# Performance work log

Measured on AMD Instinct MI355X. Metric: run time of the kernel, lower is better.

## Reference

```python
import jax, jax.numpy as jnp
import numpy as np

N = 4096
C = 8192
D = 64
MARGIN = 0.1
ALPHA = 32.0


def setup_inputs() -> dict:
    key = jax.random.key(0)
    k1, k2, k3, k4 = jax.random.split(key, 4)
    embeddings = jax.random.normal(k1, (N, D), dtype=jnp.float32)
    labels = jax.random.randint(k2, (N,), 0, C)
    # kaiming_normal_(mode='fan_out') on a (C, D) tensor -> std = sqrt(2/C)
    mean_proxies = jax.random.normal(k3, (C, D), dtype=jnp.float32) * np.sqrt(2.0 / C)
    log_variance_proxies = jax.random.normal(k4, (C, D), dtype=jnp.float32) * np.sqrt(2.0 / C)
    return {
        "embeddings": embeddings,
        "labels": labels,
        "mean_proxies": mean_proxies,
        "log_variance_proxies": log_variance_proxies,
    }


def _mls_scores(e, mu, logvar):
    """score[i,j] = -0.5 * sum_d[(e_id - mu_jd)^2 * exp(-logvar_jd) + logvar_jd].
    Expanded into GEMMs to avoid materializing the (N, C, D) broadcast tensor."""
    inv_var = jnp.exp(-logvar)                                  # (C, D)
    e2_term = (e * e) @ inv_var.T                               # (N, C)
    cross = e @ (mu * inv_var).T                                # (N, C)
    const = jnp.sum(mu * mu * inv_var + logvar, axis=1)         # (C,)
    return -0.5 * (e2_term - 2.0 * cross + const[None, :])      # (N, C)


def reference(embeddings, labels, mean_proxies, log_variance_proxies):
    score_mat = _mls_scores(embeddings, mean_proxies, log_variance_proxies)  # (N, C)
    pos_mask = jax.nn.one_hot(labels, C, dtype=score_mat.dtype)              # (N, C)

    pos_e = -ALPHA * (score_mat - MARGIN)
    neg_e = ALPHA * (score_mat + MARGIN)
    m = jnp.max(pos_e)  # NOTE: original code uses max(pos_exp) for BOTH terms
    pos_exp = jnp.exp(pos_e - m)
    neg_exp = jnp.exp(neg_e - m)

    counts = jnp.sum(pos_mask, axis=0)                   # (C,)
    num_valid = jnp.sum(counts != 0).astype(score_mat.dtype)

    pos_sim_sum = jnp.sum(jnp.where(pos_mask == 1, pos_exp, 0.0), axis=0)  # (C,)
    neg_sim_sum = jnp.sum(jnp.where(pos_mask == 0, neg_exp, 0.0), axis=0)  # (C,)

    pos_term = jnp.sum(jnp.log1p(pos_sim_sum) + m) / num_valid
    neg_term = jnp.sum(jnp.log1p(neg_sim_sum) + m) / C
    return pos_term + neg_term
```

## Files before the change

### kernel.cpp

```cpp
#include <hip/hip_runtime.h>
#include <hip/hip_bf16.h>
#include <math.h>


#define N_EMB 4096
#define C_CLS 8192
#define D_DIM 64
#define K_DIM 128

#define S2_F    23.083120654223414f
#define B2_F     4.616624130844683f
#define NEGC2_F  9.233248261689366f
#define LN2_F    0.6931471805599453f

typedef __attribute__((ext_vector_type(8))) __bf16 bf16x8;
typedef __attribute__((ext_vector_type(4))) __bf16 bf16x4;
typedef __attribute__((ext_vector_type(16))) float f32x16;
typedef __attribute__((ext_vector_type(4))) int i32x4;

__device__ __forceinline__ void async_ld16(void* lds, const void* g) {
  __builtin_amdgcn_global_load_lds(
      (__attribute__((address_space(1))) void*)g,
      (__attribute__((address_space(3))) void*)lds, 16, 0, 0);
}

__global__ void k_prep(const float* __restrict__ emb,
                       const float* __restrict__ mp,
                       const float* __restrict__ lvp,
                       __bf16* __restrict__ wsA,
                       __bf16* __restrict__ wsB,
                       float* __restrict__ constv) {
  const int wave = (int)((blockIdx.x * blockDim.x + threadIdx.x) >> 6);
  const int lane = threadIdx.x & 63;
  const int sub = lane >> 4, q = lane & 15;
  const int row = wave * 4 + sub;
  if (row < N_EMB) {
    float4 e4 = *(const float4*)&emb[row * D_DIM + q * 4];
    bf16x4 sq = {(__bf16)(e4.x * e4.x), (__bf16)(e4.y * e4.y),
                 (__bf16)(e4.z * e4.z), (__bf16)(e4.w * e4.w)};
    bf16x4 ev = {(__bf16)e4.x, (__bf16)e4.y, (__bf16)e4.z, (__bf16)e4.w};
    *(bf16x4*)&wsA[row * K_DIM + q * 4] = sq;
    *(bf16x4*)&wsA[row * K_DIM + D_DIM + q * 4] = ev;
  } else {
    const int j = row - N_EMB;
    float4 mu4 = *(const float4*)&mp[j * D_DIM + q * 4];
    float4 lv4 = *(const float4*)&lvp[j * D_DIM + q * 4];
    float iv0 = __expf(-lv4.x), iv1 = __expf(-lv4.y);
    float iv2 = __expf(-lv4.z), iv3 = __expf(-lv4.w);
    bf16x4 ivv = {(__bf16)iv0, (__bf16)iv1, (__bf16)iv2, (__bf16)iv3};
    bf16x4 mv = {(__bf16)(-2.0f * mu4.x * iv0), (__bf16)(-2.0f * mu4.y * iv1),
                 (__bf16)(-2.0f * mu4.z * iv2), (__bf16)(-2.0f * mu4.w * iv3)};
    *(bf16x4*)&wsB[j * K_DIM + q * 4] = ivv;
    *(bf16x4*)&wsB[j * K_DIM + D_DIM + q * 4] = mv;
    float t = fmaf(mu4.x * mu4.x, iv0, lv4.x)
            + fmaf(mu4.y * mu4.y, iv1, lv4.y)
            + fmaf(mu4.z * mu4.z, iv2, lv4.z)
            + fmaf(mu4.w * mu4.w, iv3, lv4.w);
    #pragma unroll
    for (int s = 8; s >= 1; s >>= 1) t += __shfl_xor(t, s);
    if (q == 0) constv[j] = t;
  }
}

__global__ __launch_bounds__(256, 2) void k_main(
    const __bf16* __restrict__ wsA, const __bf16* __restrict__ wsB,
    const float* __restrict__ constv, const int* __restrict__ labels,
    float* __restrict__ wsM, float* __restrict__ wsP, float* __restrict__ wsN) {
  __shared__ __align__(16) char As[32768];
  __shared__ __align__(16) char Bs[32768];

  const int tid = threadIdx.x;
  const int rb = blockIdx.x & 31;
  const int cb = blockIdx.x >> 5;

  const char* Ag = (const char*)(wsA + (size_t)rb * 128 * K_DIM);
  const char* Bg = (const char*)(wsB + (size_t)cb * 128 * K_DIM);
  #pragma unroll
  for (int it = 0; it < 8; ++it) {
    int L = it * 256 + tid;
    int r = L >> 4, cs = L & 15;
    int goff = r * 256 + ((cs ^ (r & 15)) << 4);
    async_ld16(As + L * 16, Ag + goff);
  }
  #pragma unroll
  for (int it = 0; it < 8; ++it) {
    int L = it * 256 + tid;
    int r = L >> 4, cs = L & 15;
    int goff = r * 256 + ((cs ^ (r & 15)) << 4);
    async_ld16(Bs + L * 16, Bg + goff);
  }
  int lab_r = 0; float cv_r = 0.f;
  if (tid < 128) {
    lab_r = labels[rb * 128 + tid];
    cv_r  = constv[cb * 128 + tid];
  }
  __syncthreads();

  const int wv = tid >> 6, lane = tid & 63;
  const int wr = wv >> 1, wc = wv & 1;
  const int l31 = lane & 31, kg = lane >> 5;
  const int l15 = lane & 15;

  f32x16 acc[2][2];
  #pragma unroll
  for (int mi = 0; mi < 2; ++mi)
    #pragma unroll
    for (int ni = 0; ni < 2; ++ni)
      #pragma unroll
      for (int r = 0; r < 16; ++r) acc[mi][ni][r] = 0.f;

  #pragma unroll
  for (int kk = 0; kk < 8; ++kk) {
    const int c = kk * 2 + kg;
    const int cofs = (c ^ l15) << 4;
    bf16x8 af[2], bfr[2];
    #pragma unroll
    for (int mi = 0; mi < 2; ++mi)
      af[mi] = *(const bf16x8*)(As + (wr * 64 + mi * 32 + l31) * 256 + cofs);
    #pragma unroll
    for (int ni = 0; ni < 2; ++ni)
      bfr[ni] = *(const bf16x8*)(Bs + (wc * 64 + ni * 32 + l31) * 256 + cofs);
    #pragma unroll
    for (int mi = 0; mi < 2; ++mi)
      #pragma unroll
      for (int ni = 0; ni < 2; ++ni)
        acc[mi][ni] = __builtin_amdgcn_mfma_f32_32x32x16_bf16(
            af[mi], bfr[ni], acc[mi][ni], 0, 0, 0);
  }

  __syncthreads();
  float* colred = (float*)As;
  int* labels_s = (int*)(As + 3072);
  float* pc_s   = (float*)(As + 3584);
  if (tid < 128) {
    labels_s[tid] = lab_r;
    pc_s[tid] = fmaf(S2_F, cv_r, B2_F);
  }
  __syncthreads();

  i32x4 labv[2][4];
  #pragma unroll
  for (int mi = 0; mi < 2; ++mi)
    #pragma unroll
    for (int g = 0; g < 4; ++g)
      labv[mi][g] = *(const i32x4*)&labels_s[wr * 64 + mi * 32 + 4 * kg + 8 * g];

  #pragma unroll
  for (int ni = 0; ni < 2; ++ni) {
    const int col_local = wc * 64 + ni * 32 + l31;
    const int gcol = cb * 128 + col_local;
    const float pcv = pc_s[col_local];
    float lmax = -1e30f;
    #pragma unroll
    for (int mi = 0; mi < 2; ++mi)
      #pragma unroll
      for (int r = 0; r < 16; ++r) {
        float pe = fmaf(S2_F, acc[mi][ni][r], pcv);
        acc[mi][ni][r] = pe;
        lmax = fmaxf(lmax, pe);
      }
    lmax = fmaxf(lmax, __shfl_xor(lmax, 32));
    const float negb = NEGC2_F - lmax;
    float ps = 0.f, ns = 0.f;
    #pragma unroll
    for (int mi = 0; mi < 2; ++mi)
      #pragma unroll
      for (int r = 0; r < 16; ++r) {
        float pe = acc[mi][ni][r];
        bool match = (labv[mi][r >> 2][r & 3] == gcol);
        float a = match ? (pe - lmax) : (negb - pe);
        float ex = exp2f(a);
        ps += match ? ex : 0.f;
        ns += match ? 0.f : ex;
      }
    ps += __shfl_xor(ps, 32);
    ns += __shfl_xor(ns, 32);
    if (kg == 0) {
      float* cr = &colred[(wr * 128 + col_local) * 3];
      cr[0] = lmax; cr[1] = ps; cr[2] = ns;
    }
  }
  __syncthreads();
  if (tid < 128) {
    const float* c0 = &colred[(0 * 128 + tid) * 3];
    const float* c1 = &colred[(1 * 128 + tid) * 3];
    float M = fmaxf(c0[0], c1[0]);
    float s0 = exp2f(c0[0] - M), s1 = exp2f(c1[0] - M);
    int gcol = cb * 128 + tid;
    wsM[rb * C_CLS + gcol] = M;
    wsP[rb * C_CLS + gcol] = fmaf(c0[1], s0, c1[1] * s1);
    wsN[rb * C_CLS + gcol] = fmaf(c0[2], s0, c1[2] * s1);
  }
}

__global__ __launch_bounds__(256) void k_red1(
    const float* __restrict__ wsM, const float* __restrict__ wsP,
    const float* __restrict__ wsN, const int* __restrict__ labels,
    float* __restrict__ Mcol, float* __restrict__ Pcol,
    float* __restrict__ Ncol, int* __restrict__ nvp) {
  __shared__ float red[8][32][3];
  __shared__ int fl[32];
  const int tid = threadIdx.x;
  const int col = tid & 31, part = tid >> 5;
  const int bx = blockIdx.x;
  const int j = bx * 32 + col;

  if (tid < 32) fl[tid] = 0;

  float m4[4];
  float M = -1e30f;
  #pragma unroll
  for (int r = 0; r < 4; ++r) {
    m4[r] = wsM[(part * 4 + r) * C_CLS + j];
    M = fmaxf(M, m4[r]);
  }
  float ps = 0.f, ns = 0.f;
  #pragma unroll
  for (int r = 0; r < 4; ++r) {
    float s = exp2f(m4[r] - M);
    ps = fmaf(wsP[(part * 4 + r) * C_CLS + j], s, ps);
    ns = fmaf(wsN[(part * 4 + r) * C_CLS + j], s, ns);
  }
  red[part][col][0] = M; red[part][col][1] = ps; red[part][col][2] = ns;
  __syncthreads();

  #pragma unroll
  for (int it = 0; it < 4; ++it) {
    int4 lb = ((const int4*)labels)[it * 256 + tid];
    if ((lb.x >> 5) == bx) fl[lb.x & 31] = 1;
    if ((lb.y >> 5) == bx) fl[lb.y & 31] = 1;
    if ((lb.z >> 5) == bx) fl[lb.z & 31] = 1;
    if ((lb.w >> 5) == bx) fl[lb.w & 31] = 1;
  }

  if (part == 0) {
    float Mx = -1e30f;
    #pragma unroll
    for (int p = 0; p < 8; ++p) Mx = fmaxf(Mx, red[p][col][0]);
    float P = 0.f, Nn = 0.f;
    #pragma unroll
    for (int p = 0; p < 8; ++p) {
      float s = exp2f(red[p][col][0] - Mx);
      P = fmaf(red[p][col][1], s, P);
      Nn = fmaf(red[p][col][2], s, Nn);
    }
    Mcol[j] = Mx; Pcol[j] = P; Ncol[j] = Nn;
  }
  __syncthreads();
  if (tid < 64) {
    int f = (tid < 32) ? fl[tid] : 0;
    #pragma unroll
    for (int s = 32; s >= 1; s >>= 1) f += __shfl_xor(f, s);
    if (tid == 0) nvp[bx] = f;
  }
}

__global__ __launch_bounds__(1024) void k_fin(
    const float* __restrict__ Mcol, const float* __restrict__ Pcol,
    const float* __restrict__ Ncol, const int* __restrict__ nvp,
    float* __restrict__ out) {
  __shared__ float sA[16], sB[16];
  __shared__ int sI[16];
  const int tid = threadIdx.x;
  const int wv = tid >> 6, lane = tid & 63;

  float colMv[8], colPv[8], colNv[8];
  #pragma unroll
  for (int k = 0; k < 8; ++k) {
    int i = k * 1024 + tid;
    colMv[k] = Mcol[i]; colPv[k] = Pcol[i]; colNv[k] = Ncol[i];
  }
  int nv = (tid < 256) ? nvp[tid] : 0;

  float gm = -1e30f;
  #pragma unroll
  for (int k = 0; k < 8; ++k) gm = fmaxf(gm, colMv[k]);
  #pragma unroll
  for (int s = 32; s >= 1; s >>= 1) {
    gm = fmaxf(gm, __shfl_xor(gm, s));
    nv += __shfl_xor(nv, s);
  }
  if (lane == 0) { sA[wv] = gm; sI[wv] = nv; }
  __syncthreads();
  if (tid == 0) {
    float mm = -1e30f; int n = 0;
    #pragma unroll
    for (int k = 0; k < 16; ++k) { mm = fmaxf(mm, sA[k]); n += sI[k]; }
    sA[0] = mm; sI[0] = n;
  }
  __syncthreads();
  const float m = sA[0];
  const int num_valid = sI[0];
  __syncthreads();
  float pt = 0.f, nt = 0.f;
  #pragma unroll
  for (int k = 0; k < 8; ++k) {
    float s = exp2f(colMv[k] - m);
    pt += log1pf(colPv[k] * s);
    nt += log1pf(colNv[k] * s);
  }
  #pragma unroll
  for (int s = 32; s >= 1; s >>= 1) {
    pt += __shfl_xor(pt, s);
    nt += __shfl_xor(nt, s);
  }
  if (lane == 0) { sA[wv] = pt; sB[wv] = nt; }
  __syncthreads();
  if (tid == 0) {
    float sp = 0.f, sn = 0.f;
    #pragma unroll
    for (int k = 0; k < 16; ++k) { sp += sA[k]; sn += sB[k]; }
    const float mn = m * LN2_F;
    out[0] = (sp + (float)C_CLS * mn) / (float)num_valid
           + (sn + (float)C_CLS * mn) / (float)C_CLS;
  }
}

extern "C" void kernel_launch(void* const* d_in, const int* in_sizes, int n_in,
                              void* d_out, int out_size, void* d_ws, size_t ws_size,
                              hipStream_t stream) {
  const float* emb    = (const float*)d_in[0];
  const int*   labels = (const int*)d_in[1];
  const float* mp     = (const float*)d_in[2];
  const float* lvp    = (const float*)d_in[3];
  float* out = (float*)d_out;

  char* ws = (char*)d_ws;
  __bf16* wsA   = (__bf16*)ws;
  __bf16* wsB   = (__bf16*)(ws + (1u << 20));
  float* constv = (float*)(ws + 3u * (1u << 20));
  float* wsM    = (float*)(ws + 3u * (1u << 20) + (1u << 15));
  float* wsP    = wsM + 32 * C_CLS;
  float* wsN    = wsP + 32 * C_CLS;
  float* Mcol   = wsN + 32 * C_CLS;
  float* Pcol   = Mcol + C_CLS;
  float* Ncol   = Pcol + C_CLS;
  int*   nvp    = (int*)(Ncol + C_CLS);

  hipLaunchKernelGGL(k_prep, dim3(768), dim3(256), 0, stream,
                     emb, mp, lvp, wsA, wsB, constv);
  hipLaunchKernelGGL(k_main, dim3((N_EMB / 128) * (C_CLS / 128)), dim3(256), 0, stream,
                     wsA, wsB, constv, labels, wsM, wsP, wsN);
  hipLaunchKernelGGL(k_red1, dim3(256), dim3(256), 0, stream,
                     wsM, wsP, wsN, labels, Mcol, Pcol, Ncol, nvp);
  hipLaunchKernelGGL(k_fin, dim3(1), dim3(1024), 0, stream,
                     Mcol, Pcol, Ncol, nvp, out);
}
```

Before: 104.5 us.

## Process four column blocks per workgroup reusing the A tile, use raw v_exp

Each k_main workgroup now loops over four consecutive 128-column class blocks while keeping its 128-row A tile resident in LDS, reloading only B per block. The next B tile is issued asynchronously after the MFMA loop, before the epilogue, so it can overlap with the exp/reduction work. Labels and per-column constants are loaded straight into registers instead of being staged through LDS. exp2f is replaced by raw v_exp_f32 inline asm, and the negative term is computed for every element with the matching element subtracted back out. The grid shrinks fourfold to 512 blocks, which lowers parallelism on a large GPU and increases register pressure. The inline v_exp_f32 also skips the denormal range handling that exp2f provides.

```diff
diff --git a/kernel.cpp b/kernel.cpp
--- a/kernel.cpp
+++ b/kernel.cpp
@@ -7,6 +7,7 @@
 #define C_CLS 8192
 #define D_DIM 64
 #define K_DIM 128
+#define NCB 4
 
 #define S2_F    23.083120654223414f
 #define B2_F     4.616624130844683f
@@ -22,6 +23,12 @@
   __builtin_amdgcn_global_load_lds(
       (__attribute__((address_space(1))) void*)g,
       (__attribute__((address_space(3))) void*)lds, 16, 0, 0);
+}
+
+__device__ __forceinline__ float fexp2(float x) {
+  float r;
+  asm("v_exp_f32 %0, %1" : "=v"(r) : "v"(x));
+  return r;
 }
 
 __global__ void k_prep(const float* __restrict__ emb,
@@ -68,13 +75,14 @@
     float* __restrict__ wsM, float* __restrict__ wsP, float* __restrict__ wsN) {
   __shared__ __align__(16) char As[32768];
   __shared__ __align__(16) char Bs[32768];
+  __shared__ float colred[2][128][3];
 
   const int tid = threadIdx.x;
-  const int rb = blockIdx.x & 31;
-  const int cb = blockIdx.x >> 5;
+  const int rb  = blockIdx.x & 31;
+  const int cbg = blockIdx.x >> 5;
 
   const char* Ag = (const char*)(wsA + (size_t)rb * 128 * K_DIM);
-  const char* Bg = (const char*)(wsB + (size_t)cb * 128 * K_DIM);
+  const char* Bgb = (const char*)(wsB + (size_t)(cbg * NCB) * 128 * K_DIM);
   #pragma unroll
   for (int it = 0; it < 8; ++it) {
     int L = it * 256 + tid;
@@ -87,109 +95,121 @@
     int L = it * 256 + tid;
     int r = L >> 4, cs = L & 15;
     int goff = r * 256 + ((cs ^ (r & 15)) << 4);
-    async_ld16(Bs + L * 16, Bg + goff);
-  }
-  int lab_r = 0; float cv_r = 0.f;
-  if (tid < 128) {
-    lab_r = labels[rb * 128 + tid];
-    cv_r  = constv[cb * 128 + tid];
-  }
-  __syncthreads();
+    async_ld16(Bs + L * 16, Bgb + goff);
+  }
 
   const int wv = tid >> 6, lane = tid & 63;
   const int wr = wv >> 1, wc = wv & 1;
   const int l31 = lane & 31, kg = lane >> 5;
   const int l15 = lane & 15;
 
-  f32x16 acc[2][2];
+  i32x4 labv[2][4];
   #pragma unroll
   for (int mi = 0; mi < 2; ++mi)
     #pragma unroll
+    for (int g = 0; g < 4; ++g)
+      labv[mi][g] = *(const i32x4*)&labels[rb * 128 + wr * 64 + mi * 32 +
+                                           4 * kg + 8 * g];
+  float cvv[NCB][2];
+  #pragma unroll
+  for (int cbi = 0; cbi < NCB; ++cbi)
+    #pragma unroll
     for (int ni = 0; ni < 2; ++ni)
-      #pragma unroll
-      for (int r = 0; r < 16; ++r) acc[mi][ni][r] = 0.f;
-
-  #pragma unroll
-  for (int kk = 0; kk < 8; ++kk) {
-    const int c = kk * 2 + kg;
-    const int cofs = (c ^ l15) << 4;
-    bf16x8 af[2], bfr[2];
+      cvv[cbi][ni] = constv[(cbg * NCB + cbi) * 128 + wc * 64 + ni * 32 + l31];
+
+  __syncthreads();
+
+  #pragma unroll
+  for (int cbi = 0; cbi < NCB; ++cbi) {
+    const int cb = cbg * NCB + cbi;
+
+    f32x16 acc[2][2];
     #pragma unroll
     for (int mi = 0; mi < 2; ++mi)
-      af[mi] = *(const bf16x8*)(As + (wr * 64 + mi * 32 + l31) * 256 + cofs);
-    #pragma unroll
-    for (int ni = 0; ni < 2; ++ni)
-      bfr[ni] = *(const bf16x8*)(Bs + (wc * 64 + ni * 32 + l31) * 256 + cofs);
-    #pragma unroll
-    for (int mi = 0; mi < 2; ++mi)
       #pragma unroll
       for (int ni = 0; ni < 2; ++ni)
-        acc[mi][ni] = __builtin_amdgcn_mfma_f32_32x32x16_bf16(
-            af[mi], bfr[ni], acc[mi][ni], 0, 0, 0);
-  }
-
-  __syncthreads();
-  float* colred = (float*)As;
-  int* labels_s = (int*)(As + 3072);
-  float* pc_s   = (float*)(As + 3584);
-  if (tid < 128) {
-    labels_s[tid] = lab_r;
-    pc_s[tid] = fmaf(S2_F, cv_r, B2_F);
-  }
-  __syncthreads();
-
-  i32x4 labv[2][4];
-  #pragma unroll
-  for (int mi = 0; mi < 2; ++mi)
-    #pragma unroll
-    for (int g = 0; g < 4; ++g)
-      labv[mi][g] = *(const i32x4*)&labels_s[wr * 64 + mi * 32 + 4 * kg + 8 * g];
-
-  #pragma unroll
-  for (int ni = 0; ni < 2; ++ni) {
-    const int col_local = wc * 64 + ni * 32 + l31;
-    const int gcol = cb * 128 + col_local;
-    const float pcv = pc_s[col_local];
-    float lmax = -1e30f;
-    #pragma unroll
-    for (int mi = 0; mi < 2; ++mi)
-      #pragma unroll
-      for (int r = 0; r < 16; ++r) {
-        float pe = fmaf(S2_F, acc[mi][ni][r], pcv);
-        acc[mi][ni][r] = pe;
-        lmax = fmaxf(lmax, pe);
+        #pragma unroll
+        for (int r = 0; r < 16; ++r) acc[mi][ni][r] = 0.f;
+
+    #pragma unroll
+    for (int kk = 0; kk < 8; ++kk) {
+      const int c = kk * 2 + kg;
+      const int cofs = (c ^ l15) << 4;
+      bf16x8 af[2], bfr[2];
+      #pragma unroll
+      for (int mi = 0; mi < 2; ++mi)
+        af[mi] = *(const bf16x8*)(As + (wr * 64 + mi * 32 + l31) * 256 + cofs);
+      #pragma unroll
+      for (int ni = 0; ni < 2; ++ni)
+        bfr[ni] = *(const bf16x8*)(Bs + (wc * 64 + ni * 32 + l31) * 256 + cofs);
+      #pragma unroll
+      for (int mi = 0; mi < 2; ++mi)
+        #pragma unroll
+        for (int ni = 0; ni < 2; ++ni)
+          acc[mi][ni] = __builtin_amdgcn_mfma_f32_32x32x16_bf16(
+              af[mi], bfr[ni], acc[mi][ni], 0, 0, 0);
+    }
+
+    __syncthreads();
+
+    if (cbi + 1 < NCB) {
+      const char* Bg = Bgb + (size_t)(cbi + 1) * 32768;
+      #pragma unroll
+      for (int it = 0; it < 8; ++it) {
+        int L = it * 256 + tid;
+        int r = L >> 4, cs = L & 15;
+        int goff = r * 256 + ((cs ^ (r & 15)) << 4);
+        async_ld16(Bs + L * 16, Bg + goff);
       }
-    lmax = fmaxf(lmax, __shfl_xor(lmax, 32));
-    const float negb = NEGC2_F - lmax;
-    float ps = 0.f, ns = 0.f;
-    #pragma unroll
-    for (int mi = 0; mi < 2; ++mi)
-      #pragma unroll
-      for (int r = 0; r < 16; ++r) {
-        float pe = acc[mi][ni][r];
-        bool match = (labv[mi][r >> 2][r & 3] == gcol);
-        float a = match ? (pe - lmax) : (negb - pe);
-        float ex = exp2f(a);
-        ps += match ? ex : 0.f;
-        ns += match ? 0.f : ex;
+    }
+
+    #pragma unroll
+    for (int ni = 0; ni < 2; ++ni) {
+      const int col_local = wc * 64 + ni * 32 + l31;
+      const int gcol = cb * 128 + col_local;
+      const float pcv = fmaf(S2_F, cvv[cbi][ni], B2_F);
+      float lmax = -1e30f;
+      #pragma unroll
+      for (int mi = 0; mi < 2; ++mi)
+        #pragma unroll
+        for (int r = 0; r < 16; ++r) {
+          float pe = fmaf(S2_F, acc[mi][ni][r], pcv);
+          acc[mi][ni][r] = pe;
+          lmax = fmaxf(lmax, pe);
+        }
+      lmax = fmaxf(lmax, __shfl_xor(lmax, 32));
+      const float negb = NEGC2_F - lmax;
+      float ps = 0.f, ns = 0.f;
+      #pragma unroll
+      for (int mi = 0; mi < 2; ++mi)
+        #pragma unroll
+        for (int r = 0; r < 16; ++r) {
+          float pe = acc[mi][ni][r];
+          float ex = fexp2(negb - pe);
+          ns += ex;
+          if (labv[mi][r >> 2][r & 3] == gcol) {
+            ns -= ex;
+            ps += fexp2(pe - lmax);
+          }
+        }
+      ps += __shfl_xor(ps, 32);
+      ns += __shfl_xor(ns, 32);
+      if (kg == 0) {
+        colred[wr][col_local][0] = lmax;
+        colred[wr][col_local][1] = ps;
+        colred[wr][col_local][2] = ns;
       }
-    ps += __shfl_xor(ps, 32);
-    ns += __shfl_xor(ns, 32);
-    if (kg == 0) {
-      float* cr = &colred[(wr * 128 + col_local) * 3];
-      cr[0] = lmax; cr[1] = ps; cr[2] = ns;
-    }
-  }
-  __syncthreads();
-  if (tid < 128) {
-    const float* c0 = &colred[(0 * 128 + tid) * 3];
-    const float* c1 = &colred[(1 * 128 + tid) * 3];
-    float M = fmaxf(c0[0], c1[0]);
-    float s0 = exp2f(c0[0] - M), s1 = exp2f(c1[0] - M);
-    int gcol = cb * 128 + tid;
-    wsM[rb * C_CLS + gcol] = M;
-    wsP[rb * C_CLS + gcol] = fmaf(c0[1], s0, c1[1] * s1);
-    wsN[rb * C_CLS + gcol] = fmaf(c0[2], s0, c1[2] * s1);
+    }
+    __syncthreads();
+    if (tid < 128) {
+      float m0 = colred[0][tid][0], m1 = colred[1][tid][0];
+      float M = fmaxf(m0, m1);
+      float s0 = fexp2(m0 - M), s1 = fexp2(m1 - M);
+      int gcol = cb * 128 + tid;
+      wsM[rb * C_CLS + gcol] = M;
+      wsP[rb * C_CLS + gcol] = fmaf(colred[0][tid][1], s0, colred[1][tid][1] * s1);
+      wsN[rb * C_CLS + gcol] = fmaf(colred[0][tid][2], s0, colred[1][tid][2] * s1);
+    }
   }
 }
 
@@ -217,7 +237,7 @@
   float ps = 0.f, ns = 0.f;
   #pragma unroll
   for (int r = 0; r < 4; ++r) {
-    float s = exp2f(m4[r] - M);
+    float s = fexp2(m4[r] - M);
     ps = fmaf(wsP[(part * 4 + r) * C_CLS + j], s, ps);
     ns = fmaf(wsN[(part * 4 + r) * C_CLS + j], s, ns);
   }
@@ -240,7 +260,7 @@
     float P = 0.f, Nn = 0.f;
     #pragma unroll
     for (int p = 0; p < 8; ++p) {
-      float s = exp2f(red[p][col][0] - Mx);
+      float s = fexp2(red[p][col][0] - Mx);
       P = fmaf(red[p][col][1], s, P);
       Nn = fmaf(red[p][col][2], s, Nn);
     }
@@ -295,7 +315,7 @@
   float pt = 0.f, nt = 0.f;
   #pragma unroll
   for (int k = 0; k < 8; ++k) {
-    float s = exp2f(colMv[k] - m);
+    float s = fexp2(colMv[k] - m);
     pt += log1pf(colPv[k] * s);
     nt += log1pf(colNv[k] * s);
   }
@@ -339,7 +359,7 @@
 
   hipLaunchKernelGGL(k_prep, dim3(768), dim3(256), 0, stream,
                      emb, mp, lvp, wsA, wsB, constv);
-  hipLaunchKernelGGL(k_main, dim3((N_EMB / 128) * (C_CLS / 128)), dim3(256), 0, stream,
+  hipLaunchKernelGGL(k_main, dim3(32 * (C_CLS / 128 / NCB)), dim3(256), 0, stream,
                      wsA, wsB, constv, labels, wsM, wsP, wsN);
   hipLaunchKernelGGL(k_red1, dim3(256), dim3(256), 0, stream,
                      wsM, wsP, wsN, labels, Mcol, Pcol, Ncol, nvp);
```

Measured after the change: 98.82 us. -5.4%, faster.
